# Kernel optimization log

Hardware: AMD Instinct MI355X
Metric: run time of the kernel (lower is better)

## Reference

```python
import jax, jax.numpy as jnp
import numpy as np

B, T, D, H, d = 2, 2048, 1024, 16, 64
INNER = H * d
SCALE = d ** -0.5


def _rope(x, inv_freq):
    # x: [B, H, T, d], interleaved rotary as in the torch module
    t = x.shape[2]
    pos = jnp.arange(t, dtype=jnp.float32)
    freqs = pos[:, None] * inv_freq[None, :]          # [T, d/2]
    cos_f, sin_f = jnp.cos(freqs), jnp.sin(freqs)
    x1, x2 = x[..., 0::2], x[..., 1::2]
    y1 = x1 * cos_f - x2 * sin_f
    y2 = x1 * sin_f + x2 * cos_f
    return jnp.stack([y1, y2], axis=-1).reshape(x.shape)


def setup_inputs() -> dict:
    key = jax.random.key(0)
    ks = jax.random.split(key, 6)
    x = jax.random.normal(ks[0], (B, T, D), jnp.float32)
    W_qkv = jax.random.normal(ks[1], (D, 3 * INNER), jnp.float32) * (D ** -0.5)
    W_out = jax.random.normal(ks[2], (INNER, D), jnp.float32) * (INNER ** -0.5)
    W_dt = jax.random.normal(ks[3], (D, H), jnp.float32) * 0.01
    b_dt = jnp.full((H,), -4.0, jnp.float32)
    W_gsp = jax.random.normal(ks[4], (D, INNER), jnp.float32) * 0.01
    b_gsp = jnp.full((INNER,), -3.0, jnp.float32)
    inv_freq = 1.0 / (10000.0 ** (jnp.arange(0, d, 2, dtype=jnp.float32) / d))
    return {"x": x, "W_qkv": W_qkv, "W_out": W_out, "W_dt": W_dt,
            "b_dt": b_dt, "W_gsp": W_gsp, "b_gsp": b_gsp, "inv_freq": inv_freq}


def reference(x, W_qkv, W_out, W_dt, b_dt, W_gsp, b_gsp, inv_freq):
    qkv = (x @ W_qkv).reshape(B, T, 3, H, d)
    Q = jnp.moveaxis(qkv[:, :, 0], 1, 2)   # [B,H,T,d]
    K = jnp.moveaxis(qkv[:, :, 1], 1, 2)
    V = jnp.moveaxis(qkv[:, :, 2], 1, 2)
    Q = _rope(Q, inv_freq)
    K = _rope(K, inv_freq)

    dt = jax.nn.softplus(x @ W_dt + b_dt)             # [B,T,H]
    gamma = jnp.moveaxis(jnp.exp(-dt), 1, 2)          # [B,H,T]

    p = jax.nn.sigmoid(x @ W_gsp + b_gsp).reshape(B, T, H, d)
    p = jnp.moveaxis(p, 1, 2)                          # [B,H,T,d]
    gamma_eff = gamma[..., None] * (1.0 - p) + p
    gamma_scalar = gamma_eff.mean(axis=-1)            # [B,H,T]
    V = V * (1.0 - p)

    log_gamma = jnp.log(jnp.clip(gamma_scalar, 1e-6, 1.0 - 1e-6))
    lgc = jnp.cumsum(log_gamma, axis=-1)              # [B,H,T]
    log_D = jnp.clip(lgc[..., :, None] - lgc[..., None, :], -20.0, 0.0)
    causal = jnp.tril(jnp.ones((T, T), jnp.float32))
    Dm = jnp.exp(log_D) * causal                      # [B,H,T,T]

    Wscore = jnp.einsum('bhtd,bhsd->bhts', Q * SCALE, K)
    A = Wscore * Dm
    Y = jnp.einsum('bhts,bhsd->bhtd', A, V)
    Y = jnp.moveaxis(Y, 1, 2).reshape(B, T, INNER)
    return Y @ W_out
```

## Files before the change

### kernel.cpp

```cpp
#include <hip/hip_runtime.h>
#include <hip/hip_bf16.h>
#include <math.h>

#define B_     2
#define T_     2048
#define D_     1024
#define H_     16
#define INNER_ 1024
#define NC_    4096
#define SCALE_ 0.125f

typedef unsigned short u16;
typedef short short8 __attribute__((ext_vector_type(8)));
typedef float f32x4 __attribute__((ext_vector_type(4)));
typedef float f32x16 __attribute__((ext_vector_type(16)));
typedef unsigned short u16x4 __attribute__((ext_vector_type(4)));
typedef unsigned int u32x2 __attribute__((ext_vector_type(2)));

__device__ __forceinline__ u16 f2bf(float x) {
  union { float f; unsigned u; } v; v.f = x;
  unsigned r = v.u + 0x7fffu + ((v.u >> 16) & 1u);
  return (u16)(r >> 16);
}
__device__ __forceinline__ float b2f(u16 x) {
  union { unsigned u; float f; } v; v.u = ((unsigned)x) << 16;
  return v.f;
}
__device__ __forceinline__ unsigned cvtpk(float lo, float hi) {
  unsigned r;
  asm("v_cvt_pk_bf16_f32 %0, %1, %2" : "=v"(r) : "v"(lo), "v"(hi));
  return r;
}
__device__ __forceinline__ void gload16(const void* g, void* l) {
  __builtin_amdgcn_global_load_lds(
      (const __attribute__((address_space(1))) void*)g,
      (__attribute__((address_space(3))) void*)l, 16, 0, 0);
}

__global__ __launch_bounds__(256) void prep_kernel(
    const float* __restrict__ x, const float* __restrict__ W_qkv,
    const float* __restrict__ W_gsp, const float* __restrict__ W_out,
    const float* __restrict__ W_dt, const float* __restrict__ inv_freq,
    u16* __restrict__ xb, u16* __restrict__ Wcombt, u16* __restrict__ Woutt,
    u16* __restrict__ Wdtb, float2* __restrict__ tab) {
  const int bid = blockIdx.x, tid = threadIdx.x;
  if (bid < 1280) {
    const float* src; u16* dst; int N, nx, ky;
    if (bid < 768)       { src = W_qkv; dst = Wcombt;                N = 3072; nx = bid % 48;          ky = bid / 48; }
    else if (bid < 1024) { src = W_gsp; dst = Wcombt + 3072 * 1024;  N = 1024; nx = (bid - 768) % 16;  ky = (bid - 768) / 16; }
    else                 { src = W_out; dst = Woutt;                 N = 1024; nx = (bid - 1024) % 16; ky = (bid - 1024) / 16; }
    __shared__ float tile[64][65];
    const int k0 = ky * 64, n0 = nx * 64;
    for (int e = tid; e < 4096; e += 256) {
      int kk = e >> 6, nn = e & 63;
      tile[kk][nn] = src[(size_t)(k0 + kk) * N + n0 + nn];
    }
    __syncthreads();
    for (int e = tid; e < 4096; e += 256) {
      int nn = e >> 6, kk = e & 63;
      dst[(size_t)(n0 + nn) * 1024 + k0 + kk] = f2bf(tile[kk][nn]);
    }
  } else if (bid < 1344) {
    int i = (bid - 1280) * 256 + tid;
    int k = i >> 4, h = i & 15;
    Wdtb[(size_t)h * D_ + k] = f2bf(W_dt[i]);
  } else if (bid < 1600) {
    int i = (bid - 1344) * 256 + tid;
    int t = i >> 5, j = i & 31;
    float s, c;
    sincosf((float)t * inv_freq[j], &s, &c);
    tab[i] = make_float2(c, s);
  } else {
    int base = (bid - 1600) * 1024 + tid;
#pragma unroll
    for (int r = 0; r < 4; ++r) {
      int i = base + r * 256;
      float4 v = *reinterpret_cast<const float4*>(x + (size_t)i * 4);
      u16x4 o; o.x = f2bf(v.x); o.y = f2bf(v.y); o.z = f2bf(v.z); o.w = f2bf(v.w);
      *reinterpret_cast<u16x4*>(xb + (size_t)i * 4) = o;
    }
  }
}

__global__ __launch_bounds__(256) void gamma_kernel(
    const u16* __restrict__ xb, const u16* __restrict__ Wdtb,
    const float* __restrict__ b_dt, float* __restrict__ gam) {
  const int row = blockIdx.x * 4 + (threadIdx.x >> 6);
  const int l = threadIdx.x & 63;
  const int h = l >> 2;
  const int kc = (l & 3) * 256;
  const short8* xp = (const short8*)(xb + (size_t)row * D_ + kc);
  const short8* wp = (const short8*)(Wdtb + h * D_ + kc);
  float s = 0.f;
#pragma unroll
  for (int i = 0; i < 32; ++i) {
    short8 xv = xp[i], wv = wp[i];
#pragma unroll
    for (int j = 0; j < 8; ++j) s += b2f((u16)xv[j]) * b2f((u16)wv[j]);
  }
  s += __shfl_xor(s, 1);
  s += __shfl_xor(s, 2);
  if ((l & 3) == 0) {
    float v = s + b_dt[h];
    float sp = (v > 20.f) ? v : log1pf(__expf(v));
    gam[row * H_ + h] = __expf(-sp);
  }
}

#define SWZG(r) ((((r) & 3) ^ (((r) >> 2) & 1)))

__device__ __forceinline__ void stage_op(const u16* __restrict__ gbase, int kt,
                                         char* ldst, int h, int tid) {
  int r = h * 128 + (tid >> 2);
  int kg = (tid & 3) ^ SWZG(r);
  gload16(gbase + (size_t)r * D_ + kt * 32 + kg * 8,
          ldst + (h * 128 + (tid >> 6) * 16) * 64);
}
__device__ __forceinline__ short8 ldfrag(const char* tile, int row, int g4) {
  return *(const short8*)(tile + row * 64 + ((g4 ^ SWZG(row)) << 4));
}

__global__ __launch_bounds__(512, 2) void gemm_big(
    const u16* __restrict__ A, const u16* __restrict__ Bt,
    u16* __restrict__ C) {
  __shared__ char lds[4 * 32768];
  const int tid = threadIdx.x;
  const int w = tid >> 6, l = tid & 63;
  const int bid = blockIdx.x;
  const int xcd = bid & 7, idx = bid >> 3;
  const int brow = (xcd >> 1) * 4 + (idx & 3);
  const int bcol = (xcd & 1) * 8 + (idx >> 2);
  const int m0 = brow * 256, n0 = bcol * 256;
  const int wr = (w >> 2) * 128, wc = (w & 3) * 64;
  const int ql = l & 15, g4 = l >> 4;

  const u16* Ag = A + (size_t)m0 * D_;
  const u16* Bg = Bt + (size_t)n0 * D_;

  f32x4 acc[8][4] = {};

#pragma unroll
  for (int t = 0; t < 3; ++t) {
    char* bufA = lds + t * 32768;
    char* bufB = bufA + 16384;
    stage_op(Ag, t, bufA, 0, tid); stage_op(Ag, t, bufA, 1, tid);
    stage_op(Bg, t, bufB, 0, tid); stage_op(Bg, t, bufB, 1, tid);
  }

  const int NT = D_ / 32;
  for (int kt = 0; kt < NT; ++kt) {
    if (kt < NT - 2)       asm volatile("s_waitcnt vmcnt(8)" ::: "memory");
    else if (kt == NT - 2) asm volatile("s_waitcnt vmcnt(4)" ::: "memory");
    else                   asm volatile("s_waitcnt vmcnt(0)" ::: "memory");
    __builtin_amdgcn_sched_barrier(0);
    __builtin_amdgcn_s_barrier();
    __builtin_amdgcn_sched_barrier(0);

    char* bufA = lds + (kt & 3) * 32768;
    char* bufB = bufA + 16384;
    char* nbufA = lds + ((kt + 3) & 3) * 32768;
    char* nbufB = nbufA + 16384;
    const bool pre = (kt + 3 < NT);

    if (pre) {
      stage_op(Ag, kt + 3, nbufA, 0, tid);
      stage_op(Ag, kt + 3, nbufA, 1, tid);
    }
    short8 bf[4];
#pragma unroll
    for (int nf = 0; nf < 4; ++nf) bf[nf] = ldfrag(bufB, wc + nf * 16 + ql, g4);
    short8 af[4];
#pragma unroll
    for (int mf = 0; mf < 4; ++mf) af[mf] = ldfrag(bufA, wr + mf * 16 + ql, g4);
    asm volatile("s_waitcnt lgkmcnt(0)" ::: "memory");
    __builtin_amdgcn_sched_barrier(0);
    __builtin_amdgcn_s_setprio(1);
#pragma unroll
    for (int mf = 0; mf < 4; ++mf)
#pragma unroll
      for (int nf = 0; nf < 4; ++nf)
        acc[mf][nf] = __builtin_amdgcn_mfma_f32_16x16x32_bf16(af[mf], bf[nf], acc[mf][nf], 0, 0, 0);
    __builtin_amdgcn_s_setprio(0);
    __builtin_amdgcn_s_barrier();

    if (pre) {
      stage_op(Bg, kt + 3, nbufB, 0, tid);
      stage_op(Bg, kt + 3, nbufB, 1, tid);
    }
    short8 af2[4];
#pragma unroll
    for (int mf = 0; mf < 4; ++mf) af2[mf] = ldfrag(bufA, wr + 64 + mf * 16 + ql, g4);
    asm volatile("s_waitcnt lgkmcnt(0)" ::: "memory");
    __builtin_amdgcn_sched_barrier(0);
    __builtin_amdgcn_s_setprio(1);
#pragma unroll
    for (int mf = 0; mf < 4; ++mf)
#pragma unroll
      for (int nf = 0; nf < 4; ++nf)
        acc[mf + 4][nf] = __builtin_amdgcn_mfma_f32_16x16x32_bf16(af2[mf], bf[nf], acc[mf + 4][nf], 0, 0, 0);
    __builtin_amdgcn_s_setprio(0);
  }

#pragma unroll
  for (int mf = 0; mf < 8; ++mf) {
#pragma unroll
    for (int r = 0; r < 4; ++r) {
      size_t row = (size_t)(m0 + wr + mf * 16 + g4 * 4 + r);
      size_t base = row * NC_ + n0 + wc + ql;
#pragma unroll
      for (int nf = 0; nf < 4; ++nf)
        C[base + nf * 16] = f2bf(acc[mf][nf][r]);
    }
  }
}

template <bool BF16OUT>
__global__ __launch_bounds__(256) void gemm_bt(
    const u16* __restrict__ A, const u16* __restrict__ Bt,
    void* __restrict__ Cv, int M, int N, int K) {
  __shared__ u16 As[2][128 * 64] __attribute__((aligned(16)));
  __shared__ u16 Bs[2][128 * 64] __attribute__((aligned(16)));
  const int tid = threadIdx.x, w = tid >> 6, l = tid & 63;
  const int rpx = (M >> 7) >> 3;
  const int bid = blockIdx.x;
  const int xcd = bid & 7, idx = bid >> 3;
  const int brow = xcd * rpx + (idx % rpx);
  const int bcol = idx / rpx;
  const int m0 = brow * 128, n0 = bcol * 128;
  const int wr = (w >> 1) * 64, wc = (w & 1) * 64;
  const int srow = l >> 3;
  const int kgrp = ((l & 7) ^ srow) * 8;

  f32x4 acc[4][4] = {};

  auto stage = [&](int kt, int bs) {
#pragma unroll
    for (int i = 0; i < 4; ++i) {
      int c = w * 4 + i;
      int row = c * 8 + srow;
      gload16(A + (size_t)(m0 + row) * K + kt * 64 + kgrp, (char*)As[bs] + c * 1024);
      gload16(Bt + (size_t)(n0 + row) * K + kt * 64 + kgrp, (char*)Bs[bs] + c * 1024);
    }
  };

  stage(0, 0);
  const int NT = K >> 6;
  for (int kt = 0; kt < NT; ++kt) {
    if (kt + 1 < NT) {
      stage(kt + 1, (kt + 1) & 1);
      asm volatile("s_waitcnt vmcnt(8)" ::: "memory");
    } else {
      asm volatile("s_waitcnt vmcnt(0)" ::: "memory");
    }
    __builtin_amdgcn_sched_barrier(0);
    __builtin_amdgcn_s_barrier();
    __builtin_amdgcn_sched_barrier(0);
    const char* Asb = (const char*)As[kt & 1];
    const char* Bsb = (const char*)Bs[kt & 1];
#pragma unroll
    for (int kk = 0; kk < 2; ++kk) {
      short8 af[4], bf[4];
#pragma unroll
      for (int i = 0; i < 4; ++i) {
        int ra = wr + i * 16 + (l & 15);
        int sa = kk * 4 + (l >> 4);
        af[i] = *(const short8*)(Asb + ra * 128 + ((sa ^ (ra & 7)) << 4));
        int rb = wc + i * 16 + (l & 15);
        bf[i] = *(const short8*)(Bsb + rb * 128 + ((sa ^ (rb & 7)) << 4));
      }
#pragma unroll
      for (int i = 0; i < 4; ++i)
#pragma unroll
        for (int j = 0; j < 4; ++j)
          acc[i][j] = __builtin_amdgcn_mfma_f32_16x16x32_bf16(af[i], bf[j], acc[i][j], 0, 0, 0);
    }
    if (kt + 1 < NT) __builtin_amdgcn_s_barrier();
  }
#pragma unroll
  for (int i = 0; i < 4; ++i) {
#pragma unroll
    for (int r = 0; r < 4; ++r) {
      size_t row = (size_t)(m0 + wr + i * 16 + (l >> 4) * 4 + r);
      size_t base = row * N + n0 + wc + (l & 15);
#pragma unroll
      for (int j = 0; j < 4; ++j) {
        if (BF16OUT) ((u16*)Cv)[base + j * 16] = f2bf(acc[i][j][r]);
        else         ((float*)Cv)[base + j * 16] = acc[i][j][r];
      }
    }
  }
}

__global__ __launch_bounds__(256) void pointwise_kernel(
    const u16* __restrict__ C, const float* __restrict__ gam,
    const float* __restrict__ b_gsp, const float2* __restrict__ tab,
    u16* __restrict__ Qb, u16* __restrict__ Kb, u16* __restrict__ Vb,
    float* __restrict__ lg) {
  const int row = blockIdx.x * 4 + (threadIdx.x >> 6);
  const int l = threadIdx.x & 63;
  const int b = row >> 11, t = row & (T_ - 1);
  const int h = l >> 2;
  const int dd0 = (l & 3) * 16;
  const int col = h * 64 + dd0;
  const size_t cb = (size_t)row * NC_;

  const float gh = gam[row * H_ + h];
  const short8* qp = (const short8*)(C + cb + col);
  const short8* kp = (const short8*)(C + cb + 1024 + col);
  const short8* vp = (const short8*)(C + cb + 2048 + col);
  const short8* pp = (const short8*)(C + cb + 3072 + col);
  short8 q0 = qp[0], q1 = qp[1];
  short8 k0 = kp[0], k1 = kp[1];
  short8 v0 = vp[0], v1 = vp[1];
  short8 pr0 = pp[0], pr1 = pp[1];

  float ge = 0.f;
  short8 vo0, vo1;
#pragma unroll
  for (int i = 0; i < 8; ++i) {
    float pv = b2f((u16)pr0[i]) + b_gsp[col + i];
    float p = 1.f / (1.f + __expf(-pv));
    ge += gh * (1.f - p) + p;
    vo0[i] = (short)f2bf(b2f((u16)v0[i]) * (1.f - p));
    float pv1 = b2f((u16)pr1[i]) + b_gsp[col + 8 + i];
    float p1 = 1.f / (1.f + __expf(-pv1));
    ge += gh * (1.f - p1) + p1;
    vo1[i] = (short)f2bf(b2f((u16)v1[i]) * (1.f - p1));
  }
  const size_t hm = (((size_t)(b * H_ + h)) * T_ + t) * 64 + dd0;
  ((short8*)(Vb + hm))[0] = vo0;
  ((short8*)(Vb + hm))[1] = vo1;

  ge += __shfl_xor(ge, 1);
  ge += __shfl_xor(ge, 2);
  if ((l & 3) == 0) {
    float gs = ge * (1.f / 64.f);
    gs = fminf(fmaxf(gs, 1e-6f), 1.f - 1e-6f);
    lg[((size_t)(b * H_ + h)) * T_ + t] = logf(gs);
  }

  short8 qo0, qo1, ko0, ko1;
  const float2* cs = tab + t * 32 + (dd0 >> 1);
#pragma unroll
  for (int m = 0; m < 4; ++m) {
    float2 c0 = cs[m];
    float qa = b2f((u16)q0[2 * m]), qb = b2f((u16)q0[2 * m + 1]);
    qo0[2 * m]     = (short)f2bf((qa * c0.x - qb * c0.y) * SCALE_);
    qo0[2 * m + 1] = (short)f2bf((qa * c0.y + qb * c0.x) * SCALE_);
    float ka = b2f((u16)k0[2 * m]), kb = b2f((u16)k0[2 * m + 1]);
    ko0[2 * m]     = (short)f2bf(ka * c0.x - kb * c0.y);
    ko0[2 * m + 1] = (short)f2bf(ka * c0.y + kb * c0.x);
    float2 c1 = cs[4 + m];
    float qa1 = b2f((u16)q1[2 * m]), qb1 = b2f((u16)q1[2 * m + 1]);
    qo1[2 * m]     = (short)f2bf((qa1 * c1.x - qb1 * c1.y) * SCALE_);
    qo1[2 * m + 1] = (short)f2bf((qa1 * c1.y + qb1 * c1.x) * SCALE_);
    float ka1 = b2f((u16)k1[2 * m]), kb1 = b2f((u16)k1[2 * m + 1]);
    ko1[2 * m]     = (short)f2bf(ka1 * c1.x - kb1 * c1.y);
    ko1[2 * m + 1] = (short)f2bf(ka1 * c1.y + kb1 * c1.x);
  }
  ((short8*)(Qb + hm))[0] = qo0; ((short8*)(Qb + hm))[1] = qo1;
  ((short8*)(Kb + hm))[0] = ko0; ((short8*)(Kb + hm))[1] = ko1;
}

__global__ __launch_bounds__(256) void scan_kernel(
    const float* __restrict__ lg, float* __restrict__ lgc) {
  const size_t base = (size_t)blockIdx.x * T_;
  const int tid = threadIdx.x;
  __shared__ float sums[256];
  float loc[8];
  float run = 0.f;
#pragma unroll
  for (int i = 0; i < 8; ++i) { run += lg[base + tid * 8 + i]; loc[i] = run; }
  sums[tid] = run;
  __syncthreads();
  if (tid == 0) {
    float r = 0.f;
    for (int i = 0; i < 256; ++i) { float v = sums[i]; sums[i] = r; r += v; }
  }
  __syncthreads();
  const float off = sums[tid];
#pragma unroll
  for (int i = 0; i < 8; ++i) lgc[base + tid * 8 + i] = off + loc[i];
}

__global__ __launch_bounds__(256) void kv_prep_kernel(
    const u16* __restrict__ Vb, const float* __restrict__ lgc,
    u16* __restrict__ Vtg) {
  const int stile = blockIdx.x;
  const int bh = blockIdx.y;
  const int tid = threadIdx.x;
  __shared__ u16 vt[64][72];
  const size_t base = ((size_t)bh * T_ + (size_t)stile * 64) * 64;
  const float* lgp = lgc + (size_t)bh * T_;
  const float lgb = lgp[stile * 64];
#pragma unroll
  for (int i = 0; i < 2; ++i) {
    int c = tid * 2 + i;
    int row = c >> 3, k8 = (c & 7) * 8;
    float beta = __expf(lgb - lgp[stile * 64 + row]);
    short8 vv = *(const short8*)(Vb + base + row * 64 + k8);
#pragma unroll
    for (int j = 0; j < 8; ++j) vt[row][k8 + j] = f2bf(b2f((u16)vv[j]) * beta);
  }
  __syncthreads();
#pragma unroll
  for (int i = 0; i < 2; ++i) {
    int c = tid * 2 + i;
    int dd = c >> 3, t8 = (c & 7) * 8;
    short8 o;
#pragma unroll
    for (int j = 0; j < 8; ++j) o[j] = (short)vt[t8 + j][dd];
    *(short8*)(Vtg + ((size_t)(bh * 32 + stile) * 64 + dd) * 64 + t8) = o;
  }
}

__global__ __launch_bounds__(256) void attn_mfma(
    const u16* __restrict__ Qb, const u16* __restrict__ Kb,
    const u16* __restrict__ Vtg, const float* __restrict__ lgc,
    u16* __restrict__ Y) {
  const int i = blockIdx.x;
  const int xcd = i & 7;
  const int half = i >> 8;
  const int r = (i >> 3) & 31;
  const int q8 = r >> 2;
  const int bh_hi = r & 3;
  const int qb = half ? (15 - q8) : q8;
  const int bh = xcd + (bh_hi << 3);
  const int b = bh >> 4, h = bh & 15;
  const int tid = threadIdx.x, w = tid >> 6, l = tid & 63;
  const int l31 = l & 31, hi = l >> 5;
  __shared__ u16 Ks[3][64 * 64] __attribute__((aligned(16)));
  __shared__ u16 Vs[3][64 * 64] __attribute__((aligned(16)));
  __shared__ u16 Ps[4][2048] __attribute__((aligned(16)));
  const u16* Qg = Qb + (size_t)bh * T_ * 64;
  const u16* Kg = Kb + (size_t)bh * T_ * 64;
  const u16* Vg = Vtg + (size_t)bh * 32 * 4096;
  const float* lgp = lgc + (size_t)bh * T_;
  const int srow = l >> 3, slot8 = l & 7;

  const int q0 = qb * 128 + w * 32;
  const int qg = q0 + l31;
  short8 qf[4];
#pragma unroll
  for (int kk = 0; kk < 4; ++kk)
    qf[kk] = *(const short8*)(Qg + (size_t)qg * 64 + kk * 16 + hi * 8);
  const float lgq = lgp[qg];
  const float lgtop = lgp[qb * 128];

  char* Pw = (char*)Ps[w];
  const int psw = l31 & 7;

  f32x16 yacc0 = {}, yacc1 = {};

  const int st0 = qb * 2 + 1;
  int s_min;
  {
    int lo = 0, hic = st0;
    while (lo < hic) {
      int mid = (lo + hic) >> 1;
      if (lgtop - lgp[mid * 64 + 63] > -20.f) hic = mid; else lo = mid + 1;
    }
    s_min = lo;
  }

  auto STAGE = [&](int s) {
    const int bs = s % 3;
#pragma unroll
    for (int i2 = 0; i2 < 2; ++i2) {
      int c = w * 2 + i2, row = c * 8 + srow;
      int kg = (slot8 ^ (row & 7)) * 8;
      gload16(Kg + (size_t)(s * 64 + row) * 64 + kg, (char*)Ks[bs] + c * 1024);
      gload16(Vg + (size_t)s * 4096 + row * 64 + kg, (char*)Vs[bs] + c * 1024);
    }
  };

  STAGE(st0);
  if (st0 - 1 >= s_min) STAGE(st0 - 1);

  for (int st = st0; st >= s_min; --st) {
    __builtin_amdgcn_s_barrier();
    if (st - 2 >= s_min) {
      STAGE(st - 2);
      asm volatile("s_waitcnt vmcnt(8)" ::: "memory");
    } else if (st - 1 >= s_min) {
      asm volatile("s_waitcnt vmcnt(4)" ::: "memory");
    } else {
      asm volatile("s_waitcnt vmcnt(0)" ::: "memory");
    }
    __builtin_amdgcn_sched_barrier(0);

    const bool allinv = (st * 64 > q0 + 31);
    if (!allinv) {
      const int bs = st % 3;
      const char* Ksb = (const char*)Ks[bs];
      const char* Vsb = (const char*)Vs[bs];
      const float alpha = __expf(lgq - lgp[st * 64]);
      const bool domask = (st * 64 + 63 > q0);
      const int qrel = qg - st * 64;
#pragma unroll
      for (int sblk = 0; sblk < 2; ++sblk) {
        f32x16 c = {};
        __builtin_amdgcn_s_setprio(1);
#pragma unroll
        for (int kk = 0; kk < 4; ++kk) {
          int row = sblk * 32 + l31;
          short8 kf = *(const short8*)(Ksb + row * 128 + (((kk * 2 + hi) ^ (row & 7)) << 4));
          c = __builtin_amdgcn_mfma_f32_32x32x16_bf16(kf, qf[kk], c, 0, 0, 0);
        }
        __builtin_amdgcn_s_setprio(0);
        if (domask) {
#pragma unroll
          for (int bq = 0; bq < 4; ++bq) {
            float p0 = c[bq * 4 + 0] * alpha, p1 = c[bq * 4 + 1] * alpha;
            float p2 = c[bq * 4 + 2] * alpha, p3 = c[bq * 4 + 3] * alpha;
            int s64 = sblk * 32 + bq * 8 + hi * 4;
            if (s64 + 0 > qrel) p0 = 0.f;
            if (s64 + 1 > qrel) p1 = 0.f;
            if (s64 + 2 > qrel) p2 = 0.f;
            if (s64 + 3 > qrel) p3 = 0.f;
            u32x2 pk; pk.x = cvtpk(p0, p1); pk.y = cvtpk(p2, p3);
            int slot = sblk * 4 + bq;
            *(u32x2*)(Pw + l31 * 128 + ((slot ^ psw) << 4) + hi * 8) = pk;
          }
        } else {
#pragma unroll
          for (int bq = 0; bq < 4; ++bq) {
            u32x2 pk;
            pk.x = cvtpk(c[bq * 4 + 0] * alpha, c[bq * 4 + 1] * alpha);
            pk.y = cvtpk(c[bq * 4 + 2] * alpha, c[bq * 4 + 3] * alpha);
            int slot = sblk * 4 + bq;
            *(u32x2*)(Pw + l31 * 128 + ((slot ^ psw) << 4) + hi * 8) = pk;
          }
        }
      }
#pragma unroll
      for (int kk = 0; kk < 4; ++kk) {
        short8 pf = *(const short8*)(Pw + l31 * 128 + (((kk * 2 + hi) ^ psw) << 4));
        short8 vf0 = *(const short8*)(Vsb + l31 * 128 + (((kk * 2 + hi) ^ (l31 & 7)) << 4));
        short8 vf1 = *(const short8*)(Vsb + (32 + l31) * 128 + (((kk * 2 + hi) ^ (l31 & 7)) << 4));
        __builtin_amdgcn_s_setprio(1);
        yacc0 = __builtin_amdgcn_mfma_f32_32x32x16_bf16(pf, vf0, yacc0, 0, 0, 0);
        yacc1 = __builtin_amdgcn_mfma_f32_32x32x16_bf16(pf, vf1, yacc1, 0, 0, 0);
        __builtin_amdgcn_s_setprio(0);
      }
    }
  }

#pragma unroll
  for (int reg = 0; reg < 16; ++reg) {
    int qrow = (reg & 3) + 8 * (reg >> 2) + 4 * hi;
    size_t rowg = (size_t)(b * T_) + qb * 128 + w * 32 + qrow;
    Y[rowg * INNER_ + h * 64 + l31] = f2bf(yacc0[reg]);
    Y[rowg * INNER_ + h * 64 + 32 + l31] = f2bf(yacc1[reg]);
  }
}

extern "C" void kernel_launch(void* const* d_in, const int* in_sizes, int n_in,
                              void* d_out, int out_size, void* d_ws, size_t ws_size,
                              hipStream_t stream) {
  const float* x        = (const float*)d_in[0];
  const float* W_qkv    = (const float*)d_in[1];
  const float* W_out    = (const float*)d_in[2];
  const float* W_dt     = (const float*)d_in[3];
  const float* b_dt     = (const float*)d_in[4];
  const float* W_gsp    = (const float*)d_in[5];
  const float* b_gsp    = (const float*)d_in[6];
  const float* inv_freq = (const float*)d_in[7];
  float* out = (float*)d_out;

  const int M = B_ * T_;
  char* p = (char*)d_ws;
  auto alloc = [&](size_t bytes) {
    char* r = p; p += (bytes + 255) & ~(size_t)255; return r;
  };
  u16*    xb    = (u16*)alloc((size_t)M * D_ * 2);
  u16*    Wcombt= (u16*)alloc((size_t)NC_ * D_ * 2);
  u16*    Woutt = (u16*)alloc((size_t)D_ * INNER_ * 2);
  u16*    Wdtb  = (u16*)alloc((size_t)H_ * D_ * 2);
  u16*    Cqkvp = (u16*)alloc((size_t)M * NC_ * 2);
  u16*    Qb    = (u16*)alloc((size_t)B_ * H_ * T_ * 64 * 2);
  u16*    Kb    = (u16*)alloc((size_t)B_ * H_ * T_ * 64 * 2);
  u16*    Vb    = (u16*)alloc((size_t)B_ * H_ * T_ * 64 * 2);
  float*  gam   = (float*)alloc((size_t)M * H_ * 4);
  float*  lg    = (float*)alloc((size_t)B_ * H_ * T_ * 4);
  float*  lgc   = (float*)alloc((size_t)B_ * H_ * T_ * 4);
  float2* tab   = (float2*)alloc((size_t)T_ * 32 * 8);
  u16*    Vtg   = Cqkvp;
  u16*    Yb    = Cqkvp + (size_t)4 * 1024 * 1024;

  prep_kernel<<<2624, 256, 0, stream>>>(x, W_qkv, W_gsp, W_out, W_dt, inv_freq,
                                        xb, Wcombt, Woutt, Wdtb, tab);
  gamma_kernel<<<M / 4, 256, 0, stream>>>(xb, Wdtb, b_dt, gam);
  gemm_big<<<256, 512, 0, stream>>>(xb, Wcombt, Cqkvp);

  pointwise_kernel<<<M / 4, 256, 0, stream>>>(Cqkvp, gam, b_gsp, tab,
                                              Qb, Kb, Vb, lg);
  scan_kernel<<<B_ * H_, 256, 0, stream>>>(lg, lgc);
  kv_prep_kernel<<<dim3(T_ / 64, B_ * H_), 256, 0, stream>>>(Vb, lgc, Vtg);

  attn_mfma<<<512, 256, 0, stream>>>(Qb, Kb, Vtg, lgc, Yb);

  gemm_bt<false><<<256, 256, 0, stream>>>(Yb, Woutt, out, M, D_, INNER_);
}
```

Baseline: 153.8 us.

## Switch big GEMM to double-buffered BK=64 tiles with XOR-swizzled LDS

Replaces the 4-stage, BK=32 LDS ring in the large QKV/gating GEMM with a 2-stage double buffer holding BK=64 tiles (128-byte rows, XOR swizzle over 8 chunks). Each iteration now issues twice as many MFMAs per barrier and drops the mid-iteration barrier and explicit lgkmcnt waits. The aim is fewer barriers and waitcnt stalls per unit of work. In exchange, prefetch depth shrinks to a single tile and the loop waits on vmcnt(0) every iteration, so global-load latency may be less well hidden.

```diff
diff --git a/kernel.cpp b/kernel.cpp
--- a/kernel.cpp
+++ b/kernel.cpp
@@ -107,23 +107,11 @@
   }
 }
 
-#define SWZG(r) ((((r) & 3) ^ (((r) >> 2) & 1)))
-
-__device__ __forceinline__ void stage_op(const u16* __restrict__ gbase, int kt,
-                                         char* ldst, int h, int tid) {
-  int r = h * 128 + (tid >> 2);
-  int kg = (tid & 3) ^ SWZG(r);
-  gload16(gbase + (size_t)r * D_ + kt * 32 + kg * 8,
-          ldst + (h * 128 + (tid >> 6) * 16) * 64);
-}
-__device__ __forceinline__ short8 ldfrag(const char* tile, int row, int g4) {
-  return *(const short8*)(tile + row * 64 + ((g4 ^ SWZG(row)) << 4));
-}
-
 __global__ __launch_bounds__(512, 2) void gemm_big(
     const u16* __restrict__ A, const u16* __restrict__ Bt,
     u16* __restrict__ C) {
-  __shared__ char lds[4 * 32768];
+  __shared__ u16 As[2][256 * 64] __attribute__((aligned(16)));
+  __shared__ u16 Bs[2][256 * 64] __attribute__((aligned(16)));
   const int tid = threadIdx.x;
   const int w = tid >> 6, l = tid & 63;
   const int bid = blockIdx.x;
@@ -131,82 +119,103 @@
   const int brow = (xcd >> 1) * 4 + (idx & 3);
   const int bcol = (xcd & 1) * 8 + (idx >> 2);
   const int m0 = brow * 256, n0 = bcol * 256;
-  const int wr = (w >> 2) * 128, wc = (w & 3) * 64;
+  const int wm = w >> 2, wn = w & 3;
   const int ql = l & 15, g4 = l >> 4;
 
   const u16* Ag = A + (size_t)m0 * D_;
   const u16* Bg = Bt + (size_t)n0 * D_;
 
+  auto STAGE_HALF = [&](const u16* __restrict__ Xg, u16* Xs, int kt, int h) {
+#pragma unroll
+    for (int c2 = 0; c2 < 2; ++c2) {
+      int row = h * 128 + c2 * 64 + w * 8 + (l >> 3);
+      int sl = (l & 7) ^ (row & 7);
+      gload16(Xg + (size_t)row * D_ + kt * 64 + sl * 8,
+              (char*)Xs + (h * 128 + c2 * 64) * 128 + w * 1024);
+    }
+  };
+  auto LDF = [&](const u16* Xs, int row, int kk) -> short8 {
+    int sl = (kk * 4 + g4) ^ (row & 7);
+    return *(const short8*)((const char*)Xs + row * 128 + sl * 16);
+  };
+
   f32x4 acc[8][4] = {};
 
-#pragma unroll
-  for (int t = 0; t < 3; ++t) {
-    char* bufA = lds + t * 32768;
-    char* bufB = bufA + 16384;
-    stage_op(Ag, t, bufA, 0, tid); stage_op(Ag, t, bufA, 1, tid);
-    stage_op(Bg, t, bufB, 0, tid); stage_op(Bg, t, bufB, 1, tid);
-  }
-
-  const int NT = D_ / 32;
+  STAGE_HALF(Ag, As[0], 0, 0); STAGE_HALF(Ag, As[0], 0, 1);
+  STAGE_HALF(Bg, Bs[0], 0, 0); STAGE_HALF(Bg, Bs[0], 0, 1);
+
+  const int NT = D_ / 64;
   for (int kt = 0; kt < NT; ++kt) {
-    if (kt < NT - 2)       asm volatile("s_waitcnt vmcnt(8)" ::: "memory");
-    else if (kt == NT - 2) asm volatile("s_waitcnt vmcnt(4)" ::: "memory");
-    else                   asm volatile("s_waitcnt vmcnt(0)" ::: "memory");
+    asm volatile("s_waitcnt vmcnt(0)" ::: "memory");
     __builtin_amdgcn_sched_barrier(0);
     __builtin_amdgcn_s_barrier();
     __builtin_amdgcn_sched_barrier(0);
 
-    char* bufA = lds + (kt & 3) * 32768;
-    char* bufB = bufA + 16384;
-    char* nbufA = lds + ((kt + 3) & 3) * 32768;
-    char* nbufB = nbufA + 16384;
-    const bool pre = (kt + 3 < NT);
+    const int bp = kt & 1;
+    const u16* Asb = As[bp];
+    const u16* Bsb = Bs[bp];
+    const bool pre = (kt + 1 < NT);
 
     if (pre) {
-      stage_op(Ag, kt + 3, nbufA, 0, tid);
-      stage_op(Ag, kt + 3, nbufA, 1, tid);
-    }
-    short8 bf[4];
-#pragma unroll
-    for (int nf = 0; nf < 4; ++nf) bf[nf] = ldfrag(bufB, wc + nf * 16 + ql, g4);
-    short8 af[4];
-#pragma unroll
-    for (int mf = 0; mf < 4; ++mf) af[mf] = ldfrag(bufA, wr + mf * 16 + ql, g4);
-    asm volatile("s_waitcnt lgkmcnt(0)" ::: "memory");
-    __builtin_amdgcn_sched_barrier(0);
+      STAGE_HALF(Ag, As[bp ^ 1], kt + 1, 0);
+      STAGE_HALF(Ag, As[bp ^ 1], kt + 1, 1);
+    }
+    short8 bf0[4], af[4];
+#pragma unroll
+    for (int nf = 0; nf < 4; ++nf) bf0[nf] = LDF(Bsb, wn * 64 + nf * 16 + ql, 0);
+#pragma unroll
+    for (int mf = 0; mf < 4; ++mf) af[mf] = LDF(Asb, wm * 128 + mf * 16 + ql, 0);
     __builtin_amdgcn_s_setprio(1);
 #pragma unroll
     for (int mf = 0; mf < 4; ++mf)
 #pragma unroll
       for (int nf = 0; nf < 4; ++nf)
-        acc[mf][nf] = __builtin_amdgcn_mfma_f32_16x16x32_bf16(af[mf], bf[nf], acc[mf][nf], 0, 0, 0);
+        acc[mf][nf] = __builtin_amdgcn_mfma_f32_16x16x32_bf16(af[mf], bf0[nf], acc[mf][nf], 0, 0, 0);
     __builtin_amdgcn_s_setprio(0);
-    __builtin_amdgcn_s_barrier();
 
     if (pre) {
-      stage_op(Bg, kt + 3, nbufB, 0, tid);
-      stage_op(Bg, kt + 3, nbufB, 1, tid);
-    }
-    short8 af2[4];
-#pragma unroll
-    for (int mf = 0; mf < 4; ++mf) af2[mf] = ldfrag(bufA, wr + 64 + mf * 16 + ql, g4);
-    asm volatile("s_waitcnt lgkmcnt(0)" ::: "memory");
-    __builtin_amdgcn_sched_barrier(0);
+      STAGE_HALF(Bg, Bs[bp ^ 1], kt + 1, 0);
+      STAGE_HALF(Bg, Bs[bp ^ 1], kt + 1, 1);
+    }
+#pragma unroll
+    for (int mf = 0; mf < 4; ++mf) af[mf] = LDF(Asb, wm * 128 + 64 + mf * 16 + ql, 0);
     __builtin_amdgcn_s_setprio(1);
 #pragma unroll
     for (int mf = 0; mf < 4; ++mf)
 #pragma unroll
       for (int nf = 0; nf < 4; ++nf)
-        acc[mf + 4][nf] = __builtin_amdgcn_mfma_f32_16x16x32_bf16(af2[mf], bf[nf], acc[mf + 4][nf], 0, 0, 0);
+        acc[mf + 4][nf] = __builtin_amdgcn_mfma_f32_16x16x32_bf16(af[mf], bf0[nf], acc[mf + 4][nf], 0, 0, 0);
     __builtin_amdgcn_s_setprio(0);
+
+#pragma unroll
+    for (int nf = 0; nf < 4; ++nf) bf0[nf] = LDF(Bsb, wn * 64 + nf * 16 + ql, 1);
+#pragma unroll
+    for (int mf = 0; mf < 4; ++mf) af[mf] = LDF(Asb, wm * 128 + mf * 16 + ql, 1);
+    __builtin_amdgcn_s_setprio(1);
+#pragma unroll
+    for (int mf = 0; mf < 4; ++mf)
+#pragma unroll
+      for (int nf = 0; nf < 4; ++nf)
+        acc[mf][nf] = __builtin_amdgcn_mfma_f32_16x16x32_bf16(af[mf], bf0[nf], acc[mf][nf], 0, 0, 0);
+    __builtin_amdgcn_s_setprio(0);
+
+#pragma unroll
+    for (int mf = 0; mf < 4; ++mf) af[mf] = LDF(Asb, wm * 128 + 64 + mf * 16 + ql, 1);
+    __builtin_amdgcn_s_setprio(1);
+#pragma unroll
+    for (int mf = 0; mf < 4; ++mf)
+#pragma unroll
+      for (int nf = 0; nf < 4; ++nf)
+        acc[mf + 4][nf] = __builtin_amdgcn_mfma_f32_16x16x32_bf16(af[mf], bf0[nf], acc[mf + 4][nf], 0, 0, 0);
+    __builtin_amdgcn_s_setprio(0);
   }
 
 #pragma unroll
   for (int mf = 0; mf < 8; ++mf) {
 #pragma unroll
     for (int r = 0; r < 4; ++r) {
-      size_t row = (size_t)(m0 + wr + mf * 16 + g4 * 4 + r);
-      size_t base = row * NC_ + n0 + wc + ql;
+      size_t row = (size_t)(m0 + wm * 128 + mf * 16 + g4 * 4 + r);
+      size_t base = row * NC_ + n0 + wn * 64 + ql;
 #pragma unroll
       for (int nf = 0; nf < 4; ++nf)
         C[base + nf * 16] = f2bf(acc[mf][nf][r]);
```

Measured after the change: 154.1 us. About the same (+0.2%).
